# Optimization experiments

Hardware: AMD Instinct MI355X
Metric: run time of the kernel (lower is better)

The kernel has to match this reference:

```python
import jax, jax.numpy as jnp
import numpy as np

NUM_ITEMS = 100000
FEAT = 64
EMB = 64
B = 16384
H = 50


def setup_inputs() -> dict:
    key = jax.random.key(0)
    ks = jax.random.split(key, 16)
    inp = {
        'hist_indices': jax.random.randint(ks[0], (B, H), 0, NUM_ITEMS),
        'hist_features': jax.random.normal(ks[1], (B, H, FEAT), dtype=jnp.float32),
        'hist_ratings': jax.random.uniform(ks[2], (B, H), dtype=jnp.float32) * 4.0 + 1.0,
        'target_indices': jax.random.randint(ks[3], (B,), 0, NUM_ITEMS),
        'target_features': jax.random.normal(ks[4], (B, FEAT), dtype=jnp.float32),
        # parameters
        'embed_table': jax.random.normal(ks[5], (NUM_ITEMS, EMB), dtype=jnp.float32) * 0.05,
        'fusion_w': jax.random.normal(ks[6], (EMB + FEAT, EMB), dtype=jnp.float32) * 0.05,
        'fusion_b': jnp.zeros((EMB,), dtype=jnp.float32),
        'w1': jax.random.normal(ks[7], (EMB * 2, 64), dtype=jnp.float32) * 0.05,
        'b1': jnp.zeros((64,), dtype=jnp.float32),
        'w2': jax.random.normal(ks[8], (64, 32), dtype=jnp.float32) * 0.05,
        'b2': jnp.zeros((32,), dtype=jnp.float32),
        'w3': jax.random.normal(ks[9], (32, 1), dtype=jnp.float32) * 0.05,
        'b3': jnp.zeros((1,), dtype=jnp.float32),
    }
    return inp


def _item_rep(idx, feats, embed_table, fusion_w, fusion_b):
    emb = embed_table[idx]  # gather: (..., EMB)
    x = jnp.concatenate([emb, feats], axis=-1)
    return jax.nn.relu(x @ fusion_w + fusion_b)


def reference(hist_indices, hist_features, hist_ratings, target_indices, target_features,
              embed_table, fusion_w, fusion_b, w1, b1, w2, b2, w3, b3):
    # user vector: weighted-sum pooling over history
    hist_reps = _item_rep(hist_indices, hist_features, embed_table, fusion_w, fusion_b)  # (B,H,EMB)
    weights = (hist_ratings - 3.0)[..., None]  # (B,H,1)
    user_vec = jnp.sum(hist_reps * weights, axis=1) / (jnp.sum(jnp.abs(weights), axis=1) + 1e-8)  # (B,EMB)
    # target representation
    target_rep = _item_rep(target_indices, target_features, embed_table, fusion_w, fusion_b)  # (B,EMB)
    # rating MLP (dropout is identity at inference)
    x = jnp.concatenate([user_vec, target_rep], axis=-1)  # (B, 2*EMB)
    h = jax.nn.relu(x @ w1 + b1)
    h = jax.nn.relu(h @ w2 + b2)
    pred = h @ w3 + b3  # (B,1)
    return pred.squeeze(-1)
```

## Files before the change

### kernel.cpp

```cpp
#include <hip/hip_runtime.h>
#include <hip/hip_bf16.h>

#define NB 16384
#define NH 50

typedef __attribute__((ext_vector_type(4))) float        f32x4;
typedef __attribute__((ext_vector_type(8))) short        s16x8;
typedef __attribute__((ext_vector_type(4))) unsigned int u32x4;


__device__ __forceinline__ unsigned rne16(float x) {
  unsigned u = __float_as_uint(x);
  return (u + 0x7FFFu + ((u >> 16) & 1u)) >> 16;
}

__device__ __forceinline__ unsigned pk_bf16(float r0, float r1) {
  __hip_bfloat162 h = __float22bfloat162_rn(make_float2(r0, r1));
  unsigned u;
  __builtin_memcpy(&u, &h, 4);
  return u;
}

__device__ __forceinline__ void cvt8t(const f32x4 a, const f32x4 b, u32x4& hi, u32x4& lo) {
  unsigned ha[8]; float r[8];
#pragma unroll
  for (int i = 0; i < 4; ++i) {
    const unsigned ua = __float_as_uint(a[i]) & 0xFFFF0000u;
    ha[i] = ua; r[i] = a[i] - __uint_as_float(ua);
  }
#pragma unroll
  for (int i = 0; i < 4; ++i) {
    const unsigned ub = __float_as_uint(b[i]) & 0xFFFF0000u;
    ha[4 + i] = ub; r[4 + i] = b[i] - __uint_as_float(ub);
  }
#pragma unroll
  for (int p = 0; p < 4; ++p) {
    hi[p] = ha[2 * p + 1] | (ha[2 * p] >> 16);
    lo[p] = pk_bf16(r[2 * p], r[2 * p + 1]);
  }
}

__global__ __launch_bounds__(256) void wprep_k(const float* __restrict__ fw,
                                               unsigned* __restrict__ bfrag) {
  const int d = blockIdx.x * 256 + threadIdx.x;
  const int j = d & 3, l = (d >> 2) & 63, f = d >> 8;
  const int sp = f & 1, nt = (f >> 1) & 3, ks = f >> 3;
  const int n  = nt * 16 + (l & 15);
  const int k0 = ks * 32 + (l >> 4) * 8 + 2 * j;
  const float w0 = fw[k0 * 64 + n], w1 = fw[(k0 + 1) * 64 + n];
  const unsigned h0 = rne16(w0), h1 = rne16(w1);
  unsigned dw;
  if (sp == 0) dw = h0 | (h1 << 16);
  else {
    const float r0 = w0 - __uint_as_float(h0 << 16);
    const float r1 = w1 - __uint_as_float(h1 << 16);
    dw = rne16(r0) | (rne16(r1) << 16);
  }
  bfrag[d] = dw;
}

__global__ __launch_bounds__(256, 3) void pool_mfma_k(
    const int* __restrict__ hidx, const float* __restrict__ hfeat,
    const float* __restrict__ hrat, const int* __restrict__ tidx,
    const float* __restrict__ tfeat, const float* __restrict__ table,
    const float* __restrict__ fb, const unsigned* __restrict__ bfrag,
    float* __restrict__ user_vec, float* __restrict__ target_rep)
{
  __shared__ u32x4 sB[2048];
  const int tid = threadIdx.x;
  {
    const u32x4* src = (const u32x4*)bfrag;
#pragma unroll
    for (int k = 0; k < 8; ++k) sB[tid + k * 256] = src[tid + k * 256];
  }

  const int l  = tid & 63;
  const int wv = tid >> 6;
  const int wave = (blockIdx.x << 2) + wv;
  const int lm = l & 15, lg = l >> 4;
  const int b0 = wave, b1 = wave + 8192;

  const int r_l = (l < NH) ? l : (NH - 1);
  int idxv0 = hidx[(size_t)b0 * NH + r_l];
  int idxv1 = hidx[(size_t)b1 * NH + r_l];
  float rat0 = (l < NH) ? (hrat[(size_t)b0 * NH + l] - 3.0f) : 0.f;
  float rat1 = (l < NH) ? (hrat[(size_t)b1 * NH + l] - 3.0f) : 0.f;
  if (l == NH) { idxv0 = tidx[b0]; idxv1 = tidx[b1]; }

  float bias[4];
#pragma unroll
  for (int nt = 0; nt < 4; ++nt) bias[nt] = fb[nt * 16 + lm];

  __syncthreads();

  float uacc[4] = {0.f, 0.f, 0.f, 0.f};
  float trep[4] = {0.f, 0.f, 0.f, 0.f};

#pragma unroll
  for (int i = 0; i < 8; ++i) {
    const int rep = i >> 2, m = i & 3;
    const int bb  = rep ? b1 : b0;
    const int mi  = rep ? idxv1 : idxv0;
    const int r   = m * 16 + lm;
    const int sel = (r <= NH) ? r : (NH - 1);
    const int idxm = __shfl(mi, sel, 64);
    const float* fp = (r < NH) ? (hfeat + ((size_t)bb * NH + r) * 64)
                    : (r == NH) ? (tfeat + (size_t)bb * 64)
                                : (hfeat + ((size_t)bb * NH + (NH - 1)) * 64);
    const float* ep = table + (size_t)idxm * 64;

    f32x4 q[8];
    q[0] = *(const f32x4*)(ep + lg * 8);
    q[1] = *(const f32x4*)(ep + lg * 8 + 4);
    q[2] = *(const f32x4*)(ep + 32 + lg * 8);
    q[3] = *(const f32x4*)(ep + 32 + lg * 8 + 4);
    q[4] = *(const f32x4*)(fp + lg * 8);
    q[5] = *(const f32x4*)(fp + lg * 8 + 4);
    q[6] = *(const f32x4*)(fp + 32 + lg * 8);
    q[7] = *(const f32x4*)(fp + 32 + lg * 8 + 4);

    u32x4 ahi[4], alo[4];
    cvt8t(q[0], q[1], ahi[0], alo[0]);
    cvt8t(q[2], q[3], ahi[1], alo[1]);
    cvt8t(q[4], q[5], ahi[2], alo[2]);
    cvt8t(q[6], q[7], ahi[3], alo[3]);

    f32x4 acc[4];
#pragma unroll
    for (int nt = 0; nt < 4; ++nt) {
      const float bv = bias[nt];
      acc[nt] = (f32x4){bv, bv, bv, bv};
    }
#pragma unroll
    for (int ks = 0; ks < 4; ++ks) {
      const s16x8 ah = __builtin_bit_cast(s16x8, ahi[ks]);
      const s16x8 al = __builtin_bit_cast(s16x8, alo[ks]);
#pragma unroll
      for (int nt = 0; nt < 4; ++nt) {
        const s16x8 bh = __builtin_bit_cast(s16x8, sB[((ks * 8 + nt * 2 + 0) * 64) + l]);
        const s16x8 bl = __builtin_bit_cast(s16x8, sB[((ks * 8 + nt * 2 + 1) * 64) + l]);
        acc[nt] = __builtin_amdgcn_mfma_f32_16x16x32_bf16(ah, bh, acc[nt], 0, 0, 0);
        acc[nt] = __builtin_amdgcn_mfma_f32_16x16x32_bf16(al, bh, acc[nt], 0, 0, 0);
        acc[nt] = __builtin_amdgcn_mfma_f32_16x16x32_bf16(ah, bl, acc[nt], 0, 0, 0);
      }
    }

    const float rw_all = rep ? rat1 : rat0;
#pragma unroll
    for (int e = 0; e < 4; ++e) {
      const int rr = m * 16 + lg * 4 + e;
      const float w = __shfl(rw_all, rr, 64);
#pragma unroll
      for (int nt = 0; nt < 4; ++nt) {
        const float repv = fmaxf(acc[nt][e], 0.f);
        uacc[nt] = fmaf(w, repv, uacc[nt]);
        if (m == 3 && e == 2) trep[nt] = repv;
      }
    }

    if (m == 3) {
      float den = fabsf(rw_all);
#pragma unroll
      for (int s = 32; s >= 1; s >>= 1) den += __shfl_xor(den, s, 64);
#pragma unroll
      for (int nt = 0; nt < 4; ++nt) {
        uacc[nt] += __shfl_xor(uacc[nt], 16, 64);
        uacc[nt] += __shfl_xor(uacc[nt], 32, 64);
      }
      const float dinv = den + 1e-8f;
      const float usel = (lg == 0) ? uacc[0] : (lg == 1) ? uacc[1]
                       : (lg == 2) ? uacc[2] : uacc[3];
      user_vec[(size_t)bb * 64 + l] = usel / dinv;
      if (l < 16) {
        float* tp = target_rep + (size_t)bb * 64 + l;
        tp[0]  = trep[0];
        tp[16] = trep[1];
        tp[32] = trep[2];
        tp[48] = trep[3];
      }
#pragma unroll
      for (int nt = 0; nt < 4; ++nt) { uacc[nt] = 0.f; trep[nt] = 0.f; }
    }

    __builtin_amdgcn_sched_barrier(0);
  }
}

__global__ __launch_bounds__(256) void mlp_k(
    const float* __restrict__ user_vec, const float* __restrict__ target_rep,
    const float* __restrict__ w1, const float* __restrict__ b1,
    const float* __restrict__ w2, const float* __restrict__ b2,
    const float* __restrict__ w3, const float* __restrict__ b3,
    float* __restrict__ out)
{
  __shared__ alignas(16) float s_w1[128 * 64];
  __shared__ alignas(16) float s_w2[64 * 32];
  __shared__ float s_w3[32];
  __shared__ alignas(16) float s_x[4][128];
  __shared__ alignas(16) float s_h1[4][64];
  const int tid = threadIdx.x;
  for (int i = tid; i < 128 * 64; i += 256) s_w1[i] = w1[i];
  for (int i = tid; i < 64 * 32;  i += 256) s_w2[i] = w2[i];
  if (tid < 32) s_w3[tid] = w3[tid];
  __syncthreads();

  const int t  = tid & 63;
  const int wv = tid >> 6;
  const int nwaves = gridDim.x << 2;
  const float b1t = b1[t];
  const float bb3 = b3[0];
  const int n2 = t & 31;
  const float b2n = b2[n2];
  for (int b = (blockIdx.x << 2) + wv; b < NB; b += nwaves) {
    s_x[wv][t]      = user_vec[(size_t)b * 64 + t];
    s_x[wv][64 + t] = target_rep[(size_t)b * 64 + t];
    float a0 = b1t, a1 = 0.f, a2 = 0.f, a3 = 0.f;
#pragma unroll
    for (int k4 = 0; k4 < 32; ++k4) {
      float4 x = *reinterpret_cast<const float4*>(&s_x[wv][k4 * 4]);
      a0 = fmaf(x.x, s_w1[(4 * k4 + 0) * 64 + t], a0);
      a1 = fmaf(x.y, s_w1[(4 * k4 + 1) * 64 + t], a1);
      a2 = fmaf(x.z, s_w1[(4 * k4 + 2) * 64 + t], a2);
      a3 = fmaf(x.w, s_w1[(4 * k4 + 3) * 64 + t], a3);
    }
    s_h1[wv][t] = fmaxf((a0 + a1) + (a2 + a3), 0.f);
    float c0 = b2n, c1 = 0.f, c2 = 0.f, c3 = 0.f;
#pragma unroll
    for (int k4 = 0; k4 < 16; ++k4) {
      float4 x = *reinterpret_cast<const float4*>(&s_h1[wv][k4 * 4]);
      c0 = fmaf(x.x, s_w2[(4 * k4 + 0) * 32 + n2], c0);
      c1 = fmaf(x.y, s_w2[(4 * k4 + 1) * 32 + n2], c1);
      c2 = fmaf(x.z, s_w2[(4 * k4 + 2) * 32 + n2], c2);
      c3 = fmaf(x.w, s_w2[(4 * k4 + 3) * 32 + n2], c3);
    }
    const float h2 = fmaxf((c0 + c1) + (c2 + c3), 0.f);
    float p = (t < 32) ? h2 * s_w3[n2] : 0.f;
#pragma unroll
    for (int m = 32; m >= 1; m >>= 1) p += __shfl_xor(p, m, 64);
    if (t == 0) out[b] = p + bb3;
  }
}

extern "C" void kernel_launch(void* const* d_in, const int* in_sizes, int n_in,
                              void* d_out, int out_size, void* d_ws, size_t ws_size,
                              hipStream_t stream) {
  const int*   hidx  = (const int*)  d_in[0];
  const float* hfeat = (const float*)d_in[1];
  const float* hrat  = (const float*)d_in[2];
  const int*   tidx  = (const int*)  d_in[3];
  const float* tfeat = (const float*)d_in[4];
  const float* table = (const float*)d_in[5];
  const float* fw    = (const float*)d_in[6];
  const float* fb    = (const float*)d_in[7];
  const float* w1    = (const float*)d_in[8];
  const float* b1    = (const float*)d_in[9];
  const float* w2    = (const float*)d_in[10];
  const float* b2    = (const float*)d_in[11];
  const float* w3    = (const float*)d_in[12];
  const float* b3    = (const float*)d_in[13];
  float* out = (float*)d_out;
  float* ws  = (float*)d_ws;
  unsigned* bfrag   = (unsigned*)ws;
  float* user_vec   = ws + 6400000;
  float* target_rep = ws + 7448576;

  hipLaunchKernelGGL(wprep_k, dim3(32), dim3(256), 0, stream, fw, bfrag);
  hipLaunchKernelGGL(pool_mfma_k, dim3(2048), dim3(256), 0, stream,
                     hidx, hfeat, hrat, tidx, tfeat, table, fb, bfrag,
                     user_vec, target_rep);
  hipLaunchKernelGGL(mlp_k, dim3(512), dim3(256), 0, stream,
                     user_vec, target_rep, w1, b1, w2, b2, w3, b3, out);
}
```

Measured before the change: 106.0 us.

## Pre-split embedding table into bf16 hi/lo and double-buffer tile loads

Adds a prep kernel that converts the whole 100k x 64 embedding table into packed bf16 hi and residual lo arrays, so the pool kernel gathers pre-split fragments instead of converting fp32 rows on the fly. The pool kernel also software-pipelines its gather: the loads for the next 16-row tile are issued before the MFMAs of the current tile run. In exchange, every call now converts the full table (about 25.6MB read and 25.6MB written), whereas the gather only touches roughly 0.8M rows. The hi part is truncated rather than rounded, with the residual captured in lo.

```diff
diff --git a/kernel.cpp b/kernel.cpp
--- a/kernel.cpp
+++ b/kernel.cpp
@@ -3,6 +3,7 @@
 
 #define NB 16384
 #define NH 50
+#define NITEMS 100000
 
 typedef __attribute__((ext_vector_type(4))) float        f32x4;
 typedef __attribute__((ext_vector_type(8))) short        s16x8;
@@ -59,10 +60,25 @@
   bfrag[d] = dw;
 }
 
+__global__ __launch_bounds__(256) void tprep_k(const float* __restrict__ table,
+                                               unsigned* __restrict__ thi,
+                                               unsigned* __restrict__ tlo) {
+  const int d = blockIdx.x * 256 + threadIdx.x;
+  if (d >= NITEMS * 32) return;
+  const float2 e = ((const float2*)table)[d];
+  const unsigned u0 = __float_as_uint(e.x) & 0xFFFF0000u;
+  const unsigned u1 = __float_as_uint(e.y) & 0xFFFF0000u;
+  thi[d] = u1 | (u0 >> 16);
+  const float r0 = e.x - __uint_as_float(u0);
+  const float r1 = e.y - __uint_as_float(u1);
+  tlo[d] = pk_bf16(r0, r1);
+}
+
 __global__ __launch_bounds__(256, 3) void pool_mfma_k(
     const int* __restrict__ hidx, const float* __restrict__ hfeat,
     const float* __restrict__ hrat, const int* __restrict__ tidx,
-    const float* __restrict__ tfeat, const float* __restrict__ table,
+    const float* __restrict__ tfeat,
+    const unsigned* __restrict__ thi, const unsigned* __restrict__ tlo,
     const float* __restrict__ fb, const unsigned* __restrict__ bfrag,
     float* __restrict__ user_vec, float* __restrict__ target_rep)
 {
@@ -93,11 +109,7 @@
 
   __syncthreads();
 
-  float uacc[4] = {0.f, 0.f, 0.f, 0.f};
-  float trep[4] = {0.f, 0.f, 0.f, 0.f};
-
-#pragma unroll
-  for (int i = 0; i < 8; ++i) {
+  auto load_tile = [&](int i, u32x4* qe, f32x4* qf) {
     const int rep = i >> 2, m = i & 3;
     const int bb  = rep ? b1 : b0;
     const int mi  = rep ? idxv1 : idxv0;
@@ -107,23 +119,40 @@
     const float* fp = (r < NH) ? (hfeat + ((size_t)bb * NH + r) * 64)
                     : (r == NH) ? (tfeat + (size_t)bb * 64)
                                 : (hfeat + ((size_t)bb * NH + (NH - 1)) * 64);
-    const float* ep = table + (size_t)idxm * 64;
-
-    f32x4 q[8];
-    q[0] = *(const f32x4*)(ep + lg * 8);
-    q[1] = *(const f32x4*)(ep + lg * 8 + 4);
-    q[2] = *(const f32x4*)(ep + 32 + lg * 8);
-    q[3] = *(const f32x4*)(ep + 32 + lg * 8 + 4);
-    q[4] = *(const f32x4*)(fp + lg * 8);
-    q[5] = *(const f32x4*)(fp + lg * 8 + 4);
-    q[6] = *(const f32x4*)(fp + 32 + lg * 8);
-    q[7] = *(const f32x4*)(fp + 32 + lg * 8 + 4);
+    const unsigned* eh = thi + (size_t)idxm * 32;
+    const unsigned* el = tlo + (size_t)idxm * 32;
+    qe[0] = *(const u32x4*)(eh + lg * 4);
+    qe[1] = *(const u32x4*)(eh + 16 + lg * 4);
+    qe[2] = *(const u32x4*)(el + lg * 4);
+    qe[3] = *(const u32x4*)(el + 16 + lg * 4);
+    qf[0] = *(const f32x4*)(fp + lg * 8);
+    qf[1] = *(const f32x4*)(fp + lg * 8 + 4);
+    qf[2] = *(const f32x4*)(fp + 32 + lg * 8);
+    qf[3] = *(const f32x4*)(fp + 32 + lg * 8 + 4);
+  };
+
+  u32x4 qeA[4], qeB[4];
+  f32x4 qfA[4], qfB[4];
+  load_tile(0, qeA, qfA);
+
+  float uacc[4] = {0.f, 0.f, 0.f, 0.f};
+  float trep[4] = {0.f, 0.f, 0.f, 0.f};
+
+#pragma unroll
+  for (int i = 0; i < 8; ++i) {
+    const int rep = i >> 2, m = i & 3;
+    u32x4* qec = (i & 1) ? qeB : qeA;
+    f32x4* qfc = (i & 1) ? qfB : qfA;
+    u32x4* qen = (i & 1) ? qeA : qeB;
+    f32x4* qfn = (i & 1) ? qfA : qfB;
 
     u32x4 ahi[4], alo[4];
-    cvt8t(q[0], q[1], ahi[0], alo[0]);
-    cvt8t(q[2], q[3], ahi[1], alo[1]);
-    cvt8t(q[4], q[5], ahi[2], alo[2]);
-    cvt8t(q[6], q[7], ahi[3], alo[3]);
+    ahi[0] = qec[0]; ahi[1] = qec[1];
+    alo[0] = qec[2]; alo[1] = qec[3];
+    cvt8t(qfc[0], qfc[1], ahi[2], alo[2]);
+    cvt8t(qfc[2], qfc[3], ahi[3], alo[3]);
+
+    if (i < 7) load_tile(i + 1, qen, qfn);
 
     f32x4 acc[4];
 #pragma unroll
@@ -159,6 +188,7 @@
     }
 
     if (m == 3) {
+      const int bb = rep ? b1 : b0;
       float den = fabsf(rw_all);
 #pragma unroll
       for (int s = 32; s >= 1; s >>= 1) den += __shfl_xor(den, s, 64);
@@ -260,13 +290,16 @@
   const float* b3    = (const float*)d_in[13];
   float* out = (float*)d_out;
   float* ws  = (float*)d_ws;
-  unsigned* bfrag   = (unsigned*)ws;
-  float* user_vec   = ws + 6400000;
-  float* target_rep = ws + 7448576;
+  unsigned* bfrag    = (unsigned*)ws;
+  unsigned* table_hi = (unsigned*)ws + 16384;
+  unsigned* table_lo = (unsigned*)ws + 3216384;
+  float* user_vec    = ws + 8000000;
+  float* target_rep  = ws + 9048576;
 
   hipLaunchKernelGGL(wprep_k, dim3(32), dim3(256), 0, stream, fw, bfrag);
+  hipLaunchKernelGGL(tprep_k, dim3(12500), dim3(256), 0, stream, table, table_hi, table_lo);
   hipLaunchKernelGGL(pool_mfma_k, dim3(2048), dim3(256), 0, stream,
-                     hidx, hfeat, hrat, tidx, tfeat, table, fb, bfrag,
+                     hidx, hfeat, hrat, tidx, tfeat, table_hi, table_lo, fb, bfrag,
                      user_vec, target_rep);
   hipLaunchKernelGGL(mlp_k, dim3(512), dim3(256), 0, stream,
                      user_vec, target_rep, w1, b1, w2, b2, w3, b3, out);
```

Result: slower. 112.9 us (+6.5%).

## Precompute projected embedding table and prefetch next history tile in pool kernel

Applied to the files above, without the earlier changes.

Adds a kernel that multiplies the whole 100k-row embedding table by the embedding half of the fusion weight once, storing a projected table. The pooling kernel then gathers projected rows and only runs the feature half of the MFMA matmul, halving its matmul and conversion work. It also double-buffers the feature and gathered-row loads for the next tile. The cost is an extra pass over the full 25.6MB table plus a 25.6MB write, which is more than the roughly 52MB of gathered rows it replaces in total, so the trade depends on MFMA and latency savings.

```diff
diff --git a/kernel.cpp b/kernel.cpp
--- a/kernel.cpp
+++ b/kernel.cpp
@@ -3,6 +3,7 @@
 
 #define NB 16384
 #define NH 50
+#define NITEMS 100000
 
 typedef __attribute__((ext_vector_type(4))) float        f32x4;
 typedef __attribute__((ext_vector_type(8))) short        s16x8;
@@ -59,19 +60,67 @@
   bfrag[d] = dw;
 }
 
+__global__ __launch_bounds__(256) void femb_k(const float* __restrict__ table,
+                                              const unsigned* __restrict__ bfrag,
+                                              float* __restrict__ femb) {
+  __shared__ u32x4 sB[1024];
+  const int tid = threadIdx.x;
+  {
+    const u32x4* src = (const u32x4*)bfrag;
+#pragma unroll
+    for (int k = 0; k < 4; ++k) sB[tid + k * 256] = src[tid + k * 256];
+  }
+  const int l = tid & 63, wv = tid >> 6;
+  const int w = blockIdx.x * 4 + wv;
+  const int lm = l & 15, lg = l >> 4;
+  __syncthreads();
+  if (w >= NITEMS / 16) return;
+
+  const float* tp = table + (size_t)(w * 16 + lm) * 64;
+  f32x4 q0 = *(const f32x4*)(tp + lg * 8);
+  f32x4 q1 = *(const f32x4*)(tp + lg * 8 + 4);
+  f32x4 q2 = *(const f32x4*)(tp + 32 + lg * 8);
+  f32x4 q3 = *(const f32x4*)(tp + 32 + lg * 8 + 4);
+  u32x4 ahi[2], alo[2];
+  cvt8t(q0, q1, ahi[0], alo[0]);
+  cvt8t(q2, q3, ahi[1], alo[1]);
+
+  f32x4 acc[4];
+#pragma unroll
+  for (int nt = 0; nt < 4; ++nt) acc[nt] = (f32x4){0.f, 0.f, 0.f, 0.f};
+#pragma unroll
+  for (int ks = 0; ks < 2; ++ks) {
+    const s16x8 ah = __builtin_bit_cast(s16x8, ahi[ks]);
+    const s16x8 al = __builtin_bit_cast(s16x8, alo[ks]);
+#pragma unroll
+    for (int nt = 0; nt < 4; ++nt) {
+      const s16x8 bh = __builtin_bit_cast(s16x8, sB[((ks * 8 + nt * 2 + 0) * 64) + l]);
+      const s16x8 bl = __builtin_bit_cast(s16x8, sB[((ks * 8 + nt * 2 + 1) * 64) + l]);
+      acc[nt] = __builtin_amdgcn_mfma_f32_16x16x32_bf16(ah, bh, acc[nt], 0, 0, 0);
+      acc[nt] = __builtin_amdgcn_mfma_f32_16x16x32_bf16(al, bh, acc[nt], 0, 0, 0);
+      acc[nt] = __builtin_amdgcn_mfma_f32_16x16x32_bf16(ah, bl, acc[nt], 0, 0, 0);
+    }
+  }
+#pragma unroll
+  for (int e = 0; e < 4; ++e)
+#pragma unroll
+    for (int nt = 0; nt < 4; ++nt)
+      femb[(size_t)(w * 16 + lg * 4 + e) * 64 + lm + 16 * nt] = acc[nt][e];
+}
+
 __global__ __launch_bounds__(256, 3) void pool_mfma_k(
     const int* __restrict__ hidx, const float* __restrict__ hfeat,
     const float* __restrict__ hrat, const int* __restrict__ tidx,
-    const float* __restrict__ tfeat, const float* __restrict__ table,
+    const float* __restrict__ tfeat, const float* __restrict__ femb,
     const float* __restrict__ fb, const unsigned* __restrict__ bfrag,
     float* __restrict__ user_vec, float* __restrict__ target_rep)
 {
-  __shared__ u32x4 sB[2048];
+  __shared__ u32x4 sB[1024];
   const int tid = threadIdx.x;
   {
-    const u32x4* src = (const u32x4*)bfrag;
-#pragma unroll
-    for (int k = 0; k < 8; ++k) sB[tid + k * 256] = src[tid + k * 256];
+    const u32x4* src = ((const u32x4*)bfrag) + 1024;
+#pragma unroll
+    for (int k = 0; k < 4; ++k) sB[tid + k * 256] = src[tid + k * 256];
   }
 
   const int l  = tid & 63;
@@ -93,37 +142,51 @@
 
   __syncthreads();
 
-  float uacc[4] = {0.f, 0.f, 0.f, 0.f};
-  float trep[4] = {0.f, 0.f, 0.f, 0.f};
-
-#pragma unroll
-  for (int i = 0; i < 8; ++i) {
+  auto load_tile = [&](int i, f32x4* qf, float* g) {
     const int rep = i >> 2, m = i & 3;
     const int bb  = rep ? b1 : b0;
     const int mi  = rep ? idxv1 : idxv0;
     const int r   = m * 16 + lm;
-    const int sel = (r <= NH) ? r : (NH - 1);
-    const int idxm = __shfl(mi, sel, 64);
     const float* fp = (r < NH) ? (hfeat + ((size_t)bb * NH + r) * 64)
                     : (r == NH) ? (tfeat + (size_t)bb * 64)
                                 : (hfeat + ((size_t)bb * NH + (NH - 1)) * 64);
-    const float* ep = table + (size_t)idxm * 64;
-
-    f32x4 q[8];
-    q[0] = *(const f32x4*)(ep + lg * 8);
-    q[1] = *(const f32x4*)(ep + lg * 8 + 4);
-    q[2] = *(const f32x4*)(ep + 32 + lg * 8);
-    q[3] = *(const f32x4*)(ep + 32 + lg * 8 + 4);
-    q[4] = *(const f32x4*)(fp + lg * 8);
-    q[5] = *(const f32x4*)(fp + lg * 8 + 4);
-    q[6] = *(const f32x4*)(fp + 32 + lg * 8);
-    q[7] = *(const f32x4*)(fp + 32 + lg * 8 + 4);
-
-    u32x4 ahi[4], alo[4];
-    cvt8t(q[0], q[1], ahi[0], alo[0]);
-    cvt8t(q[2], q[3], ahi[1], alo[1]);
-    cvt8t(q[4], q[5], ahi[2], alo[2]);
-    cvt8t(q[6], q[7], ahi[3], alo[3]);
+    qf[0] = *(const f32x4*)(fp + lg * 8);
+    qf[1] = *(const f32x4*)(fp + lg * 8 + 4);
+    qf[2] = *(const f32x4*)(fp + 32 + lg * 8);
+    qf[3] = *(const f32x4*)(fp + 32 + lg * 8 + 4);
+#pragma unroll
+    for (int e = 0; e < 4; ++e) {
+      const int rr = m * 16 + lg * 4 + e;
+      const int se = (rr <= NH) ? rr : (NH - 1);
+      const int ide = __shfl(mi, se, 64);
+      const float* gp = femb + (size_t)ide * 64 + lm;
+      g[e * 4 + 0] = gp[0];
+      g[e * 4 + 1] = gp[16];
+      g[e * 4 + 2] = gp[32];
+      g[e * 4 + 3] = gp[48];
+    }
+  };
+
+  f32x4 qfA[4], qfB[4];
+  float gA[16], gB[16];
+  load_tile(0, qfA, gA);
+
+  float uacc[4] = {0.f, 0.f, 0.f, 0.f};
+  float trep[4] = {0.f, 0.f, 0.f, 0.f};
+
+#pragma unroll
+  for (int i = 0; i < 8; ++i) {
+    const int rep = i >> 2, m = i & 3;
+    f32x4* qfc = (i & 1) ? qfB : qfA;
+    float*  gc = (i & 1) ? gB  : gA;
+    f32x4* qfn = (i & 1) ? qfA : qfB;
+    float*  gn = (i & 1) ? gA  : gB;
+
+    u32x4 ahi[2], alo[2];
+    cvt8t(qfc[0], qfc[1], ahi[0], alo[0]);
+    cvt8t(qfc[2], qfc[3], ahi[1], alo[1]);
+
+    if (i < 7) load_tile(i + 1, qfn, gn);
 
     f32x4 acc[4];
 #pragma unroll
@@ -132,7 +195,7 @@
       acc[nt] = (f32x4){bv, bv, bv, bv};
     }
 #pragma unroll
-    for (int ks = 0; ks < 4; ++ks) {
+    for (int ks = 0; ks < 2; ++ks) {
       const s16x8 ah = __builtin_bit_cast(s16x8, ahi[ks]);
       const s16x8 al = __builtin_bit_cast(s16x8, alo[ks]);
 #pragma unroll
@@ -152,13 +215,14 @@
       const float w = __shfl(rw_all, rr, 64);
 #pragma unroll
       for (int nt = 0; nt < 4; ++nt) {
-        const float repv = fmaxf(acc[nt][e], 0.f);
+        const float repv = fmaxf(acc[nt][e] + gc[e * 4 + nt], 0.f);
         uacc[nt] = fmaf(w, repv, uacc[nt]);
         if (m == 3 && e == 2) trep[nt] = repv;
       }
     }
 
     if (m == 3) {
+      const int bb = rep ? b1 : b0;
       float den = fabsf(rw_all);
 #pragma unroll
       for (int s = 32; s >= 1; s >>= 1) den += __shfl_xor(den, s, 64);
@@ -261,12 +325,15 @@
   float* out = (float*)d_out;
   float* ws  = (float*)d_ws;
   unsigned* bfrag   = (unsigned*)ws;
-  float* user_vec   = ws + 6400000;
-  float* target_rep = ws + 7448576;
+  float* femb       = ws + 16384;
+  float* user_vec   = ws + 8000000;
+  float* target_rep = ws + 9048576;
 
   hipLaunchKernelGGL(wprep_k, dim3(32), dim3(256), 0, stream, fw, bfrag);
+  hipLaunchKernelGGL(femb_k, dim3((NITEMS / 16 + 3) / 4), dim3(256), 0, stream,
+                     table, bfrag, femb);
   hipLaunchKernelGGL(pool_mfma_k, dim3(2048), dim3(256), 0, stream,
-                     hidx, hfeat, hrat, tidx, tfeat, table, fb, bfrag,
+                     hidx, hfeat, hrat, tidx, tfeat, femb, fb, bfrag,
                      user_vec, target_rep);
   hipLaunchKernelGGL(mlp_k, dim3(512), dim3(256), 0, stream,
                      user_vec, target_rep, w1, b1, w2, b2, w3, b3, out);
```

Measured after the change: 111.6 us. 1.05x slower.
